# Kernel tuning notes

Measured on AMD Instinct MI355X. Metric: run time of the kernel, lower is better.

## Reference

```python
import jax, jax.numpy as jnp
import numpy as np

T = 4096          # num tokens
HID = 2048        # hidden_size
HQ = 32           # num q heads
HKV = 8           # num kv heads
G = HQ // HKV     # GQA group size
D = 128           # head_dim (q/k)
DV = 96           # v_head_dim
W = 512           # sliding window (= query block size)
THETA = 1e6
Q_SIZE, K_SIZE, V_SIZE = HQ * D, HKV * D, HKV * DV


def setup_inputs() -> dict:
    key = jax.random.key(0)
    k1, k2, k3, k4 = jax.random.split(key, 4)
    positions = jnp.arange(T, dtype=jnp.int32)
    hidden_states = jax.random.normal(k1, (T, HID), dtype=jnp.float32)
    qkv_w = jax.random.normal(k2, (Q_SIZE + K_SIZE + V_SIZE, HID), dtype=jnp.float32) * (HID ** -0.5)
    o_w = jax.random.normal(k3, (HID, HQ * DV), dtype=jnp.float32) * ((HQ * DV) ** -0.5)
    sink_bias = jax.random.normal(k4, (HQ,), dtype=jnp.float32)
    return {"positions": positions, "hidden_states": hidden_states,
            "qkv_w": qkv_w, "o_w": o_w, "sink_bias": sink_bias}


def _rope(x, positions):
    # neox-style rotate-half RoPE on full head_dim (partial_rotary_factor=1.0)
    half = D // 2
    inv_freq = 1.0 / (THETA ** (jnp.arange(0, half, dtype=jnp.float32) / half))
    ang = positions.astype(jnp.float32)[:, None] * inv_freq[None, :]   # [T, D/2]
    cos = jnp.cos(ang)[:, None, :]
    sin = jnp.sin(ang)[:, None, :]
    x1, x2 = x[..., :half], x[..., half:]
    return jnp.concatenate([x1 * cos - x2 * sin, x2 * cos + x1 * sin], axis=-1)


def _swa_with_sink(q, k, v, sink_bias):
    # q: [T, HKV, G, D], k: [T, HKV, D], v: [T, HKV, DV]
    nb = T // W
    scale = D ** -0.5
    qb = q.reshape(nb, W, HKV, G, D)
    # per query block i, keys/values from global span [(i-1)*W, (i+1)*W)
    k_pad = jnp.pad(k, ((W, 0), (0, 0), (0, 0)))
    v_pad = jnp.pad(v, ((W, 0), (0, 0), (0, 0)))
    idx = jnp.arange(nb)[:, None] * W + jnp.arange(2 * W)[None, :]     # [nb, 2W]
    k_ext = k_pad[idx]                                                 # [nb, 2W, HKV, D]
    v_ext = v_pad[idx]                                                 # [nb, 2W, HKV, DV]
    # mask: rel = t - j in [0, W); exclude left-pad keys (key_pos < 0)
    r = jnp.arange(W)[:, None]
    c = jnp.arange(2 * W)[None, :]
    rel = W + r - c                                                    # [W, 2W]
    key_pos = (jnp.arange(nb)[:, None, None] - 1) * W + c[None]        # [nb, W(1), 2W]
    mask = (rel >= 0) & (rel < W) & (key_pos >= 0)                     # [nb, W, 2W]
    scores = jnp.einsum('nrkgd,nckd->nkgrc', qb, k_ext) * scale        # [nb,HKV,G,W,2W]
    scores = jnp.where(mask[:, None, None, :, :], scores, -jnp.inf)
    sink = jnp.broadcast_to(sink_bias.reshape(HKV, G)[None, :, :, None, None],
                            (nb, HKV, G, W, 1))
    logits = jnp.concatenate([scores, sink], axis=-1)                  # [...,2W+1]
    p = jax.nn.softmax(logits, axis=-1)[..., :-1]                      # drop sink column
    out = jnp.einsum('nkgrc,nckd->nrkgd', p, v_ext)                    # [nb,W,HKV,G,DV]
    return out.reshape(T, HQ * DV)


def reference(positions, hidden_states, qkv_w, o_w, sink_bias):
    qkv = hidden_states @ qkv_w.T                                      # [T, Q+K+V]
    q, k, v = jnp.split(qkv, [Q_SIZE, Q_SIZE + K_SIZE], axis=-1)
    q = q.reshape(T, HQ, D)
    k = k.reshape(T, HKV, D)
    v = v.reshape(T, HKV, DV)
    q = _rope(q, positions).reshape(T, HKV, G, D)
    k = _rope(k, positions)
    attn = _swa_with_sink(q, k, v, sink_bias)                          # [T, HQ*DV]
    return attn @ o_w.T                                                # [T, HID]
```

## Files before the change

### kernel.cpp

```cpp
#include <hip/hip_runtime.h>
#include <hip/hip_bf16.h>
#include <stdint.h>

#define T_SEQ 4096
#define HIDDEN 2048
#define NQH 32
#define NKVH 8
#define DH 128
#define DVH 96
#define WWIN 512
#define QKVN 5888
#define KOFF 4096
#define VOFF 5120
#define ATTN 3072
#define QSCALE 0.08838834764831845f

typedef uint16_t u16;
typedef uint32_t u32;
typedef __bf16 bfrag8 __attribute__((ext_vector_type(8)));
typedef float f32x4v __attribute__((ext_vector_type(4)));

__device__ __forceinline__ u16 f2bf(float x) {
  u32 u = __float_as_uint(x);
  return (u16)((u + 0x7fffu + ((u >> 16) & 1u)) >> 16);
}
__device__ __forceinline__ float bf2f(u16 v) { return __uint_as_float(((u32)v) << 16); }

__global__ void cvt_kernel(const float* __restrict__ in, u16* __restrict__ out, int n4) {
  int i = blockIdx.x * blockDim.x + threadIdx.x;
  int st = gridDim.x * blockDim.x;
  for (; i < n4; i += st) {
    float4 v = ((const float4*)in)[i];
    ushort4 o;
    o.x = f2bf(v.x); o.y = f2bf(v.y); o.z = f2bf(v.z); o.w = f2bf(v.w);
    ((ushort4*)out)[i] = o;
  }
}

template<int OUT_F32>
__global__ __launch_bounds__(256) void gemm_nt(const u16* __restrict__ A,
                                               const u16* __restrict__ B,
                                               void* __restrict__ Cp,
                                               int M, int N, int K) {
  __shared__ u16 Asm[128 * 32];
  __shared__ u16 Bsm[128 * 32];
  const int tid = threadIdx.x;
  const int wv = tid >> 6, lane = tid & 63;
  const int bm = blockIdx.x * 128, bn = blockIdx.y * 128;
  const int wm = (wv >> 1) * 64, wn = (wv & 1) * 64;
  const int srow = lane >> 2;
  const int scol = (lane & 3) * 8;
  const int fr = lane & 15, fk = (lane >> 4) * 8;
  f32x4v acc[4][4];
#pragma unroll
  for (int i = 0; i < 4; i++)
#pragma unroll
    for (int j = 0; j < 4; j++) acc[i][j] = {0.f, 0.f, 0.f, 0.f};

  for (int kt = 0; kt < K; kt += 32) {
    __syncthreads();
#pragma unroll
    for (int c = 0; c < 2; c++) {
      const int ci = wv * 2 + c;
      const u16* ga = A + (size_t)(bm + ci * 16 + srow) * K + kt + scol;
      const u16* gb = B + (size_t)(bn + ci * 16 + srow) * K + kt + scol;
      __builtin_amdgcn_global_load_lds((const __attribute__((address_space(1))) u32*)ga,
                                       (__attribute__((address_space(3))) u32*)(Asm + ci * 512),
                                       16, 0, 0);
      __builtin_amdgcn_global_load_lds((const __attribute__((address_space(1))) u32*)gb,
                                       (__attribute__((address_space(3))) u32*)(Bsm + ci * 512),
                                       16, 0, 0);
    }
    __syncthreads();
    bfrag8 af[4], bf[4];
#pragma unroll
    for (int i = 0; i < 4; i++) af[i] = *(const bfrag8*)(Asm + (wm + i * 16 + fr) * 32 + fk);
#pragma unroll
    for (int j = 0; j < 4; j++) bf[j] = *(const bfrag8*)(Bsm + (wn + j * 16 + fr) * 32 + fk);
#pragma unroll
    for (int i = 0; i < 4; i++)
#pragma unroll
      for (int j = 0; j < 4; j++)
        acc[i][j] = __builtin_amdgcn_mfma_f32_16x16x32_bf16(af[i], bf[j], acc[i][j], 0, 0, 0);
  }
  const int orow = (lane >> 4) * 4, ocol = lane & 15;
#pragma unroll
  for (int i = 0; i < 4; i++)
#pragma unroll
    for (int j = 0; j < 4; j++) {
      size_t base = (size_t)(bm + wm + i * 16 + orow) * N + (size_t)(bn + wn + j * 16 + ocol);
#pragma unroll
      for (int r = 0; r < 4; r++) {
        if (OUT_F32) ((float*)Cp)[base + (size_t)r * N] = acc[i][j][r];
        else         ((u16*)Cp)[base + (size_t)r * N] = f2bf(acc[i][j][r]);
      }
    }
}

__global__ void rope_kernel(u16* __restrict__ qkv, const int* __restrict__ pos) {
  int gid = blockIdx.x * 256 + threadIdx.x;
  int d = gid & 63;
  int r = gid >> 6;
  int hh = r % 40;
  int t = r / 40;
  if (t >= T_SEQ) return;
  int off = (hh < 32) ? hh * 128 : KOFF + (hh - 32) * 128;
  u16* p = qkv + (size_t)t * QKVN + off + d;
  float x1 = bf2f(p[0]);
  float x2 = bf2f(p[64]);
  float inv_freq = exp2f(-(float)d * 0.3114307588956852f);
  float ang = (float)pos[t] * inv_freq;
  float c = cosf(ang), s = sinf(ang);
  float y1 = x1 * c - x2 * s;
  float y2 = x2 * c + x1 * s;
  if (hh < 32) { y1 *= QSCALE; y2 *= QSCALE; }
  p[0] = f2bf(y1);
  p[64] = f2bf(y2);
}

__global__ __launch_bounds__(256) void vt_kernel(const u16* __restrict__ qkv,
                                                 u16* __restrict__ vt) {
  __shared__ u16 tile[64][100];
  const int t0 = blockIdx.x * 64;
  const int hk = blockIdx.y;
  const int tid = threadIdx.x;
#pragma unroll
  for (int i = 0; i < 3; i++) {
    int idx = i * 256 + tid;
    int row = idx / 12, ch = idx % 12;
    const u16* g = qkv + (size_t)(t0 + row) * QKVN + VOFF + hk * DVH + ch * 8;
    uint2 a = *(const uint2*)g;
    uint2 b = *(const uint2*)(g + 4);
    *(uint2*)&tile[row][ch * 8] = a;
    *(uint2*)&tile[row][ch * 8 + 4] = b;
  }
  __syncthreads();
#pragma unroll
  for (int i = 0; i < 3; i++) {
    int idx = i * 256 + tid;
    int dv = idx >> 3, tc = (idx & 7) * 8;
    union { uint4 v4; u16 s[8]; } o;
#pragma unroll
    for (int j = 0; j < 8; j++) o.s[j] = tile[tc + j][dv];
    *(uint4*)(vt + (((size_t)(hk * 96 + dv)) << 12) + t0 + tc) = o.v4;
  }
}

__global__ __launch_bounds__(256, 2) void attn_mfma(const u16* __restrict__ qkv,
                                                    const u16* __restrict__ vt,
                                                    const float* __restrict__ sink_bias,
                                                    u16* __restrict__ attn_out) {
  __shared__ u16 k_lds[64 * 128];
  __shared__ u16 v_lds[96 * 64];
  __shared__ u16 p_lds[4][2048];

  const int tid = threadIdx.x;
  const int wv = tid >> 6;
  const int lane = tid & 63;
  const int g = lane >> 4;
  const int c = lane & 15;
  const int t0 = blockIdx.x * 32;
  const int hk = blockIdx.y;
  const int h = hk * 4 + wv;

  bfrag8 qf[2][4];
#pragma unroll
  for (int m = 0; m < 2; m++)
#pragma unroll
    for (int kf = 0; kf < 4; kf++)
      qf[m][kf] = *(const bfrag8*)(qkv + (size_t)(t0 + m * 16 + c) * QKVN + h * DH + kf * 32 + g * 8);

  f32x4v acc_o[2][6];
#pragma unroll
  for (int m = 0; m < 2; m++)
#pragma unroll
    for (int n = 0; n < 6; n++) acc_o[m][n] = {0.f, 0.f, 0.f, 0.f};

  const float sb = sink_bias[h];
  float m_run[2][4], l_run[2][4];
#pragma unroll
  for (int m = 0; m < 2; m++)
#pragma unroll
    for (int r = 0; r < 4; r++) { m_run[m][r] = sb; l_run[m][r] = 1.0f; }

  int cb0 = t0 - (WWIN - 1);
  cb0 = (cb0 < 0) ? 0 : (cb0 & ~63);

  for (int cb = cb0; cb < t0 + 32; cb += 64) {
    __syncthreads();
#pragma unroll
    for (int it = 0; it < 4; it++) {
      int dest = it * 4096 + tid * 16;
      int row = dest >> 8;
      int src = dest ^ ((row & 7) << 4);
      const u16* gp = qkv + (size_t)(cb + row) * QKVN + KOFF + hk * DH + ((src & 255) >> 1);
      __builtin_amdgcn_global_load_lds((const __attribute__((address_space(1))) u32*)gp,
                                       (__attribute__((address_space(3))) u32*)((char*)k_lds + dest),
                                       16, 0, 0);
    }
#pragma unroll
    for (int it = 0; it < 3; it++) {
      int dest = it * 4096 + tid * 16;
      int row = dest >> 7;
      int src = dest ^ ((row & 7) << 4);
      const u16* gp = vt + (((size_t)(hk * 96 + row)) << 12) + cb + ((src & 127) >> 1);
      __builtin_amdgcn_global_load_lds((const __attribute__((address_space(1))) u32*)gp,
                                       (__attribute__((address_space(3))) u32*)((char*)v_lds + dest),
                                       16, 0, 0);
    }
    __syncthreads();

    f32x4v s[2][4];
#pragma unroll
    for (int m = 0; m < 2; m++)
#pragma unroll
      for (int n = 0; n < 4; n++) s[m][n] = {0.f, 0.f, 0.f, 0.f};
#pragma unroll
    for (int kf = 0; kf < 4; kf++) {
      bfrag8 kb[4];
#pragma unroll
      for (int n = 0; n < 4; n++) {
        int key = n * 16 + c;
        int byt = ((key << 8) + (kf << 6) + (g << 4)) ^ ((key & 7) << 4);
        kb[n] = *(const bfrag8*)((const char*)k_lds + byt);
      }
#pragma unroll
      for (int m = 0; m < 2; m++)
#pragma unroll
        for (int n = 0; n < 4; n++)
          s[m][n] = __builtin_amdgcn_mfma_f32_16x16x32_bf16(qf[m][kf], kb[n], s[m][n], 0, 0, 0);
    }

    if ((cb + 63 > t0) || (cb + WWIN < t0 + 32)) {
#pragma unroll
      for (int m = 0; m < 2; m++)
#pragma unroll
        for (int n = 0; n < 4; n++)
#pragma unroll
          for (int r = 0; r < 4; r++) {
            int rel = (t0 + m * 16 + g * 4 + r) - (cb + n * 16 + c);
            if (!(rel >= 0 && rel < WWIN)) s[m][n][r] = -3.0e38f;
          }
    }

    float corr[2][4];
#pragma unroll
    for (int m = 0; m < 2; m++)
#pragma unroll
      for (int r = 0; r < 4; r++) {
        float v0 = fmaxf(fmaxf(s[m][0][r], s[m][1][r]), fmaxf(s[m][2][r], s[m][3][r]));
        v0 = fmaxf(v0, __shfl_xor(v0, 1));
        v0 = fmaxf(v0, __shfl_xor(v0, 2));
        v0 = fmaxf(v0, __shfl_xor(v0, 4));
        v0 = fmaxf(v0, __shfl_xor(v0, 8));
        float mn = fmaxf(m_run[m][r], v0);
        corr[m][r] = __expf(m_run[m][r] - mn);
        m_run[m][r] = mn;
        float p0 = __expf(s[m][0][r] - mn);
        float p1 = __expf(s[m][1][r] - mn);
        float p2 = __expf(s[m][2][r] - mn);
        float p3 = __expf(s[m][3][r] - mn);
        s[m][0][r] = p0; s[m][1][r] = p1; s[m][2][r] = p2; s[m][3][r] = p3;
        float rs = p0 + p1 + p2 + p3;
        rs += __shfl_xor(rs, 1);
        rs += __shfl_xor(rs, 2);
        rs += __shfl_xor(rs, 4);
        rs += __shfl_xor(rs, 8);
        l_run[m][r] = l_run[m][r] * corr[m][r] + rs;
      }
#pragma unroll
    for (int m = 0; m < 2; m++)
#pragma unroll
      for (int n = 0; n < 6; n++)
#pragma unroll
      for (int r = 0; r < 4; r++) acc_o[m][n][r] *= corr[m][r];

#pragma unroll
    for (int m = 0; m < 2; m++)
#pragma unroll
      for (int n = 0; n < 4; n++) {
        u32 lo = (u32)f2bf(s[m][n][0]) | ((u32)f2bf(s[m][n][1]) << 16);
        u32 hi = (u32)f2bf(s[m][n][2]) | ((u32)f2bf(s[m][n][3]) << 16);
        int byt = ((m * 2 + (n >> 1)) << 10) | (g << 3) | ((c & 3) << 5) |
                  (((c >> 2) & 1) << 9) | ((((n & 1) * 2) + (c >> 3)) << 7);
        uint2 u; u.x = lo; u.y = hi;
        *(uint2*)((char*)&p_lds[wv][0] + byt) = u;
      }

#pragma unroll
    for (int ks = 0; ks < 2; ks++) {
      bfrag8 pa[2];
#pragma unroll
      for (int m = 0; m < 2; m++) {
        union { bfrag8 v; u16 s16[8]; } u;
#pragma unroll
        for (int j = 0; j < 4; j++) {
          int e = ((m * 2 + ks) << 9) + c + j * 16 + g * 64;
          u.s16[j] = p_lds[wv][e];
          u.s16[4 + j] = p_lds[wv][e + 256];
        }
        pa[m] = u.v;
      }
#pragma unroll
      for (int n = 0; n < 6; n++) {
        int dv = n * 16 + c;
        int byt = ((dv << 7) + (ks << 6) + (g << 4)) ^ ((dv & 7) << 4);
        bfrag8 vb = *(const bfrag8*)((const char*)v_lds + byt);
#pragma unroll
        for (int m = 0; m < 2; m++)
          acc_o[m][n] = __builtin_amdgcn_mfma_f32_16x16x32_bf16(pa[m], vb, acc_o[m][n], 0, 0, 0);
      }
    }
  }

#pragma unroll
  for (int m = 0; m < 2; m++) {
    float inv[4];
#pragma unroll
    for (int r = 0; r < 4; r++) inv[r] = 1.0f / l_run[m][r];
#pragma unroll
    for (int n = 0; n < 6; n++)
#pragma unroll
      for (int r = 0; r < 4; r++) {
        int tq = t0 + m * 16 + g * 4 + r;
        attn_out[(size_t)tq * ATTN + h * DVH + n * 16 + c] = f2bf(acc_o[m][n][r] * inv[r]);
      }
  }
}

extern "C" void kernel_launch(void* const* d_in, const int* in_sizes, int n_in,
                              void* d_out, int out_size, void* d_ws, size_t ws_size,
                              hipStream_t stream) {
  const int* positions = (const int*)d_in[0];
  const float* hidden = (const float*)d_in[1];
  const float* qkv_w = (const float*)d_in[2];
  const float* o_w = (const float*)d_in[3];
  const float* sink = (const float*)d_in[4];
  char* ws = (char*)d_ws;

  u16* hs_bf   = (u16*)(ws + 0);
  u16* w1_bf   = (u16*)(ws + 16777216);
  u16* attn_bf = (u16*)(ws + 0);
  u16* vt_buf  = (u16*)(ws + 25165824);
  u16* w2_bf   = (u16*)(ws + 40894464);
  u16* qkv_bf  = (u16*)(ws + 53477376);

  cvt_kernel<<<dim3(1024), dim3(256), 0, stream>>>(hidden, hs_bf, 8388608 / 4);
  cvt_kernel<<<dim3(1024), dim3(256), 0, stream>>>(qkv_w, w1_bf, 12058624 / 4);
  cvt_kernel<<<dim3(1024), dim3(256), 0, stream>>>(o_w, w2_bf, 6291456 / 4);

  gemm_nt<0><<<dim3(32, 46), dim3(256), 0, stream>>>(hs_bf, w1_bf, (void*)qkv_bf,
                                                     T_SEQ, QKVN, HIDDEN);
  rope_kernel<<<dim3(40960), dim3(256), 0, stream>>>(qkv_bf, positions);
  vt_kernel<<<dim3(T_SEQ / 64, NKVH), dim3(256), 0, stream>>>(qkv_bf, vt_buf);
  attn_mfma<<<dim3(T_SEQ / 32, NKVH), dim3(256), 0, stream>>>(qkv_bf, vt_buf, sink, attn_bf);
  gemm_nt<1><<<dim3(32, 16), dim3(256), 0, stream>>>(attn_bf, w2_bf, d_out,
                                                     T_SEQ, HIDDEN, ATTN);
}
```

Before: 349.0 us.

## Add triple-buffered direct-to-LDS pipelined GEMM for QKV and output projections

Adds a new GEMM kernel with 512 threads and 256-row tiles. It uses global_load_lds to copy tiles straight into XOR-swizzled shared memory, keeps three buffers in flight with explicit vmcnt waits, raises wave priority around the MFMA blocks, and remaps workgroup IDs across XCDs. Both projection GEMMs use it, with a fallback to the old kernel if the dynamic LDS attribute cannot be set. The aim is to hide global memory latency and cut LDS bank conflicts and register-staging overhead, at the cost of large LDS use (up to 96KB) and more complex synchronisation.

```diff
diff --git a/kernel.cpp b/kernel.cpp
--- a/kernel.cpp
+++ b/kernel.cpp
@@ -35,6 +35,141 @@
     o.x = f2bf(v.x); o.y = f2bf(v.y); o.z = f2bf(v.z); o.w = f2bf(v.w);
     ((ushort4*)out)[i] = o;
   }
+}
+
+template<int WN, int OUT_F32>
+__global__ __launch_bounds__(512, 2) void gemm_pipe(const u16* __restrict__ A,
+                                                    const u16* __restrict__ B,
+                                                    void* __restrict__ Cp,
+                                                    int M, int N, int K, int nbm) {
+  constexpr int BN = WN * 64;
+  constexpr int WM = 8 / WN;
+  constexpr int MF = 16 / WM;
+  constexpr int ASZ = 8192;
+  constexpr int BSZ = BN * 32;
+  constexpr int BUFSZ = ASZ + BSZ;
+  constexpr int AIN = 2;
+  constexpr int BIN = (WN == 4) ? 2 : 1;
+  constexpr int LPT = AIN + BIN;
+
+  extern __shared__ u16 lds[];
+
+  const int tid = threadIdx.x;
+  const int w = tid >> 6, lane = tid & 63;
+  const int wr = w / WN, wc = w % WN;
+  const int fr = lane & 15, kg = lane >> 4;
+
+  const int nwg = gridDim.x;
+  int bid = (int)blockIdx.x;
+  if ((nwg & 7) == 0) bid = (bid & 7) * (nwg >> 3) + (bid >> 3);
+  const int bm = (bid % nbm) * 256;
+  const int bn = (bid / nbm) * BN;
+
+  const int NT = K >> 5;
+
+  f32x4v acc[MF][4];
+#pragma unroll
+  for (int m = 0; m < MF; m++)
+#pragma unroll
+    for (int n = 0; n < 4; n++) acc[m][n] = {0.f, 0.f, 0.f, 0.f};
+
+  auto stageA = [&](int t) {
+    u16* dst = lds + (t % 3) * BUFSZ;
+#pragma unroll
+    for (int i = 0; i < AIN; i++) {
+      int D = (w * AIN + i) * 1024 + lane * 16;
+      int srow = D >> 7;
+      int Dx = D ^ ((srow & 7) << 4);
+      int c = (Dx >> 1) & 63;
+      int m = 2 * srow + (c >> 5);
+      int k = c & 31;
+      const u16* src = A + (size_t)(bm + m) * K + (t << 5) + k;
+      __builtin_amdgcn_global_load_lds((const __attribute__((address_space(1))) u32*)src,
+                                       (__attribute__((address_space(3))) u32*)((char*)dst + D),
+                                       16, 0, 0);
+    }
+  };
+  auto stageB = [&](int t) {
+    u16* dst = lds + (t % 3) * BUFSZ + ASZ;
+#pragma unroll
+    for (int i = 0; i < BIN; i++) {
+      int D = (w * BIN + i) * 1024 + lane * 16;
+      int srow = D >> 7;
+      int Dx = D ^ ((srow & 7) << 4);
+      int c = (Dx >> 1) & 63;
+      int m = 2 * srow + (c >> 5);
+      int k = c & 31;
+      const u16* src = B + (size_t)(bn + m) * K + (t << 5) + k;
+      __builtin_amdgcn_global_load_lds((const __attribute__((address_space(1))) u32*)src,
+                                       (__attribute__((address_space(3))) u32*)((char*)dst + D),
+                                       16, 0, 0);
+    }
+  };
+
+  stageA(0); stageB(0);
+  stageA(1); stageB(1);
+
+  for (int t = 0; t < NT; ++t) {
+    const u16* At = lds + (t % 3) * BUFSZ;
+    const u16* Bt = At + ASZ;
+    if (t + 1 < NT) asm volatile("s_waitcnt vmcnt(%0)" :: "n"(LPT));
+    else            asm volatile("s_waitcnt vmcnt(0)");
+    asm volatile("s_barrier" ::: "memory");
+
+    bfrag8 bfr[4];
+#pragma unroll
+    for (int n = 0; n < 4; n++) {
+      int nr = wc * 64 + n * 16 + fr;
+      int byt = (((nr >> 1) << 7) + ((nr & 1) << 6) + (kg << 4)) ^ (((nr >> 1) & 7) << 4);
+      bfr[n] = *(const bfrag8*)((const char*)Bt + byt);
+    }
+    bfrag8 afr[MF / 2];
+#pragma unroll
+    for (int m = 0; m < MF / 2; m++) {
+      int mr = wr * (MF * 16) + m * 16 + fr;
+      int byt = (((mr >> 1) << 7) + ((mr & 1) << 6) + (kg << 4)) ^ (((mr >> 1) & 7) << 4);
+      afr[m] = *(const bfrag8*)((const char*)At + byt);
+    }
+    if (t + 2 < NT) stageA(t + 2);
+    __builtin_amdgcn_s_setprio(1);
+#pragma unroll
+    for (int m = 0; m < MF / 2; m++)
+#pragma unroll
+      for (int n = 0; n < 4; n++)
+        acc[m][n] = __builtin_amdgcn_mfma_f32_16x16x32_bf16(afr[m], bfr[n], acc[m][n], 0, 0, 0);
+    __builtin_amdgcn_s_setprio(0);
+    asm volatile("s_barrier" ::: "memory");
+
+    bfrag8 afr2[MF / 2];
+#pragma unroll
+    for (int m = 0; m < MF / 2; m++) {
+      int mr = wr * (MF * 16) + (m + MF / 2) * 16 + fr;
+      int byt = (((mr >> 1) << 7) + ((mr & 1) << 6) + (kg << 4)) ^ (((mr >> 1) & 7) << 4);
+      afr2[m] = *(const bfrag8*)((const char*)At + byt);
+    }
+    if (t + 2 < NT) stageB(t + 2);
+    __builtin_amdgcn_s_setprio(1);
+#pragma unroll
+    for (int m = 0; m < MF / 2; m++)
+#pragma unroll
+      for (int n = 0; n < 4; n++)
+        acc[m + MF / 2][n] = __builtin_amdgcn_mfma_f32_16x16x32_bf16(afr2[m], bfr[n], acc[m + MF / 2][n], 0, 0, 0);
+    __builtin_amdgcn_s_setprio(0);
+  }
+
+  const int rb = bm + wr * (MF * 16);
+  const int cb = bn + wc * 64;
+#pragma unroll
+  for (int m = 0; m < MF; m++)
+#pragma unroll
+    for (int n = 0; n < 4; n++) {
+      size_t base = (size_t)(rb + m * 16 + kg * 4) * N + cb + n * 16 + fr;
+#pragma unroll
+      for (int r = 0; r < 4; r++) {
+        if (OUT_F32) ((float*)Cp)[base + (size_t)r * N] = acc[m][n][r];
+        else         ((u16*)Cp)[base + (size_t)r * N] = f2bf(acc[m][n][r]);
+      }
+    }
 }
 
 template<int OUT_F32>
@@ -345,15 +480,31 @@
   u16* w2_bf   = (u16*)(ws + 40894464);
   u16* qkv_bf  = (u16*)(ws + 53477376);
 
+  bool pipeOk =
+    (hipFuncSetAttribute((const void*)&gemm_pipe<4, 0>,
+                         hipFuncAttributeMaxDynamicSharedMemorySize, 98304) == hipSuccess) &&
+    (hipFuncSetAttribute((const void*)&gemm_pipe<2, 1>,
+                         hipFuncAttributeMaxDynamicSharedMemorySize, 73728) == hipSuccess);
+
   cvt_kernel<<<dim3(1024), dim3(256), 0, stream>>>(hidden, hs_bf, 8388608 / 4);
   cvt_kernel<<<dim3(1024), dim3(256), 0, stream>>>(qkv_w, w1_bf, 12058624 / 4);
   cvt_kernel<<<dim3(1024), dim3(256), 0, stream>>>(o_w, w2_bf, 6291456 / 4);
 
-  gemm_nt<0><<<dim3(32, 46), dim3(256), 0, stream>>>(hs_bf, w1_bf, (void*)qkv_bf,
-                                                     T_SEQ, QKVN, HIDDEN);
+  if (pipeOk)
+    gemm_pipe<4, 0><<<dim3(368), dim3(512), 98304, stream>>>(hs_bf, w1_bf, (void*)qkv_bf,
+                                                             T_SEQ, QKVN, HIDDEN, 16);
+  else
+    gemm_nt<0><<<dim3(32, 46), dim3(256), 0, stream>>>(hs_bf, w1_bf, (void*)qkv_bf,
+                                                       T_SEQ, QKVN, HIDDEN);
+
   rope_kernel<<<dim3(40960), dim3(256), 0, stream>>>(qkv_bf, positions);
   vt_kernel<<<dim3(T_SEQ / 64, NKVH), dim3(256), 0, stream>>>(qkv_bf, vt_buf);
   attn_mfma<<<dim3(T_SEQ / 32, NKVH), dim3(256), 0, stream>>>(qkv_bf, vt_buf, sink, attn_bf);
-  gemm_nt<1><<<dim3(32, 16), dim3(256), 0, stream>>>(attn_bf, w2_bf, d_out,
-                                                     T_SEQ, HIDDEN, ATTN);
-}
+
+  if (pipeOk)
+    gemm_pipe<2, 1><<<dim3(256), dim3(512), 73728, stream>>>(attn_bf, w2_bf, d_out,
+                                                             T_SEQ, HIDDEN, ATTN, 16);
+  else
+    gemm_nt<1><<<dim3(32, 16), dim3(256), 0, stream>>>(attn_bf, w2_bf, d_out,
+                                                       T_SEQ, HIDDEN, ATTN);
+}
```

After: 322.8 us. 7.5% less time.

## Add triple-buffered 256x128 GEMM with 32x32 MFMA for both projections

Applied to the files above, without the earlier changes.

Adds a new GEMM kernel with 256x128 tiles, 512 threads, and K-steps of 64. It triple-buffers LDS tiles loaded asynchronously with global_load_lds, using a swizzled layout and a partial vmcnt wait so the next tile's load overlaps compute. It also uses the 32x32x16 MFMA, s_setprio around the MFMA bursts, and an XCD-aware block remap. The QKV and output projections use it when 144KB of dynamic LDS can be set, and fall back to the old kernel otherwise. In exchange it needs a large LDS footprint (with launch_bounds(512,2)) and does a hipFuncSetAttribute call on every launch.

```diff
diff --git a/kernel.cpp b/kernel.cpp
--- a/kernel.cpp
+++ b/kernel.cpp
@@ -19,12 +19,18 @@
 typedef uint32_t u32;
 typedef __bf16 bfrag8 __attribute__((ext_vector_type(8)));
 typedef float f32x4v __attribute__((ext_vector_type(4)));
+typedef float f32x16 __attribute__((ext_vector_type(16)));
 
 __device__ __forceinline__ u16 f2bf(float x) {
   u32 u = __float_as_uint(x);
   return (u16)((u + 0x7fffu + ((u >> 16) & 1u)) >> 16);
 }
 __device__ __forceinline__ float bf2f(u16 v) { return __uint_as_float(((u32)v) << 16); }
+
+__device__ __forceinline__ void gload16(const u16* src, char* ldst) {
+  __builtin_amdgcn_global_load_lds((const __attribute__((address_space(1))) u32*)src,
+                                   (__attribute__((address_space(3))) u32*)ldst, 16, 0, 0);
+}
 
 __global__ void cvt_kernel(const float* __restrict__ in, u16* __restrict__ out, int n4) {
   int i = blockIdx.x * blockDim.x + threadIdx.x;
@@ -35,6 +41,127 @@
     o.x = f2bf(v.x); o.y = f2bf(v.y); o.z = f2bf(v.z); o.w = f2bf(v.w);
     ((ushort4*)out)[i] = o;
   }
+}
+
+template<int OUT_F32>
+__global__ __launch_bounds__(512, 2) void gemm_v3(const u16* __restrict__ A,
+                                                  const u16* __restrict__ B,
+                                                  void* __restrict__ Cp,
+                                                  int M, int N, int K, int nbm) {
+  extern __shared__ char lds[];
+  const int tid = threadIdx.x;
+  const int w = tid >> 6, lane = tid & 63;
+  const int wr = w >> 1, wc = w & 1;
+  const int r5 = lane & 31, kg = lane >> 5;
+
+  const int nwg = gridDim.x;
+  int bid = (int)blockIdx.x;
+  if ((nwg & 7) == 0) bid = (bid & 7) * (nwg >> 3) + (bid >> 3);
+  const int bm = (bid % nbm) * 256;
+  const int bn = (bid / nbm) * 128;
+  const int NT = K >> 6;
+
+  f32x16 acc[2][2];
+#pragma unroll
+  for (int mb = 0; mb < 2; mb++)
+#pragma unroll
+    for (int nb = 0; nb < 2; nb++)
+#pragma unroll
+      for (int i = 0; i < 16; i++) acc[mb][nb][i] = 0.f;
+
+  const int q = r5 * 128 + ((kg ^ (r5 & 7)) << 4);
+
+  auto stageA = [&](int t) {
+    char* dst = lds + (t % 3) * 49152;
+    const u16* Abase = A + (size_t)bm * K + ((size_t)t << 6);
+#pragma unroll
+    for (int i = 0; i < 4; i++) {
+      int D = (w * 4 + i) * 1024 + lane * 16;
+      int row = D >> 7;
+      int kb = (D ^ ((row & 7) << 4)) & 127;
+      gload16(Abase + (size_t)row * K + (kb >> 1), dst + D);
+    }
+  };
+  auto stageB = [&](int t) {
+    char* dst = lds + (t % 3) * 49152 + 32768;
+    const u16* Bbase = B + (size_t)bn * K + ((size_t)t << 6);
+#pragma unroll
+    for (int i = 0; i < 2; i++) {
+      int D = (w * 2 + i) * 1024 + lane * 16;
+      int row = D >> 7;
+      int kb = (D ^ ((row & 7) << 4)) & 127;
+      gload16(Bbase + (size_t)row * K + (kb >> 1), dst + D);
+    }
+  };
+
+  stageA(0); stageB(0);
+
+  for (int t = 0; t < NT; ++t) {
+    const char* Ab = lds + (t % 3) * 49152 + wr * 8192;
+    const char* Bb = lds + (t % 3) * 49152 + 32768 + wc * 8192;
+    if (t + 1 < NT) {
+      stageA(t + 1);
+      stageB(t + 1);
+      asm volatile("s_waitcnt vmcnt(6)");
+    } else {
+      asm volatile("s_waitcnt vmcnt(0)");
+    }
+    asm volatile("s_barrier" ::: "memory");
+
+    bfrag8 af[2][2], bf[2][2];
+#pragma unroll
+    for (int ks = 0; ks < 2; ks++) {
+#pragma unroll
+      for (int mb = 0; mb < 2; mb++)
+        af[mb][ks] = *(const bfrag8*)(Ab + mb * 4096 + (q ^ (ks << 5)));
+#pragma unroll
+      for (int nb = 0; nb < 2; nb++)
+        bf[nb][ks] = *(const bfrag8*)(Bb + nb * 4096 + (q ^ (ks << 5)));
+    }
+    __builtin_amdgcn_s_setprio(1);
+#pragma unroll
+    for (int ks = 0; ks < 2; ks++)
+#pragma unroll
+      for (int mb = 0; mb < 2; mb++)
+#pragma unroll
+        for (int nb = 0; nb < 2; nb++)
+          acc[mb][nb] = __builtin_amdgcn_mfma_f32_32x32x16_bf16(af[mb][ks], bf[nb][ks], acc[mb][nb], 0, 0, 0);
+    __builtin_amdgcn_s_setprio(0);
+
+    bfrag8 af2[2][2], bf2[2][2];
+#pragma unroll
+    for (int ks = 0; ks < 2; ks++) {
+#pragma unroll
+      for (int mb = 0; mb < 2; mb++)
+        af2[mb][ks] = *(const bfrag8*)(Ab + mb * 4096 + (q ^ ((ks + 2) << 5)));
+#pragma unroll
+      for (int nb = 0; nb < 2; nb++)
+        bf2[nb][ks] = *(const bfrag8*)(Bb + nb * 4096 + (q ^ ((ks + 2) << 5)));
+    }
+    __builtin_amdgcn_s_setprio(1);
+#pragma unroll
+    for (int ks = 0; ks < 2; ks++)
+#pragma unroll
+      for (int mb = 0; mb < 2; mb++)
+#pragma unroll
+        for (int nb = 0; nb < 2; nb++)
+          acc[mb][nb] = __builtin_amdgcn_mfma_f32_32x32x16_bf16(af2[mb][ks], bf2[nb][ks], acc[mb][nb], 0, 0, 0);
+    __builtin_amdgcn_s_setprio(0);
+  }
+
+  const int rb0 = bm + wr * 64;
+  const int cb0 = bn + wc * 64;
+#pragma unroll
+  for (int mb = 0; mb < 2; mb++)
+#pragma unroll
+    for (int nb = 0; nb < 2; nb++)
+#pragma unroll
+      for (int i = 0; i < 16; i++) {
+        int rowl = (i & 3) + 8 * (i >> 2) + 4 * kg;
+        size_t off = (size_t)(rb0 + mb * 32 + rowl) * N + cb0 + nb * 32 + r5;
+        if (OUT_F32) ((float*)Cp)[off] = acc[mb][nb][i];
+        else         ((u16*)Cp)[off] = f2bf(acc[mb][nb][i]);
+      }
 }
 
 template<int OUT_F32>
@@ -64,12 +191,8 @@
       const int ci = wv * 2 + c;
       const u16* ga = A + (size_t)(bm + ci * 16 + srow) * K + kt + scol;
       const u16* gb = B + (size_t)(bn + ci * 16 + srow) * K + kt + scol;
-      __builtin_amdgcn_global_load_lds((const __attribute__((address_space(1))) u32*)ga,
-                                       (__attribute__((address_space(3))) u32*)(Asm + ci * 512),
-                                       16, 0, 0);
-      __builtin_amdgcn_global_load_lds((const __attribute__((address_space(1))) u32*)gb,
-                                       (__attribute__((address_space(3))) u32*)(Bsm + ci * 512),
-                                       16, 0, 0);
+      gload16(ga, (char*)(Asm + ci * 512));
+      gload16(gb, (char*)(Bsm + ci * 512));
     }
     __syncthreads();
     bfrag8 af[4], bf[4];
@@ -194,9 +317,7 @@
       int row = dest >> 8;
       int src = dest ^ ((row & 7) << 4);
       const u16* gp = qkv + (size_t)(cb + row) * QKVN + KOFF + hk * DH + ((src & 255) >> 1);
-      __builtin_amdgcn_global_load_lds((const __attribute__((address_space(1))) u32*)gp,
-                                       (__attribute__((address_space(3))) u32*)((char*)k_lds + dest),
-                                       16, 0, 0);
+      gload16(gp, (char*)k_lds + dest);
     }
 #pragma unroll
     for (int it = 0; it < 3; it++) {
@@ -204,9 +325,7 @@
       int row = dest >> 7;
       int src = dest ^ ((row & 7) << 4);
       const u16* gp = vt + (((size_t)(hk * 96 + row)) << 12) + cb + ((src & 127) >> 1);
-      __builtin_amdgcn_global_load_lds((const __attribute__((address_space(1))) u32*)gp,
-                                       (__attribute__((address_space(3))) u32*)((char*)v_lds + dest),
-                                       16, 0, 0);
+      gload16(gp, (char*)v_lds + dest);
     }
     __syncthreads();
 
@@ -345,15 +464,31 @@
   u16* w2_bf   = (u16*)(ws + 40894464);
   u16* qkv_bf  = (u16*)(ws + 53477376);
 
+  bool v3Ok =
+    (hipFuncSetAttribute((const void*)&gemm_v3<0>,
+                         hipFuncAttributeMaxDynamicSharedMemorySize, 147456) == hipSuccess) &&
+    (hipFuncSetAttribute((const void*)&gemm_v3<1>,
+                         hipFuncAttributeMaxDynamicSharedMemorySize, 147456) == hipSuccess);
+
   cvt_kernel<<<dim3(1024), dim3(256), 0, stream>>>(hidden, hs_bf, 8388608 / 4);
   cvt_kernel<<<dim3(1024), dim3(256), 0, stream>>>(qkv_w, w1_bf, 12058624 / 4);
   cvt_kernel<<<dim3(1024), dim3(256), 0, stream>>>(o_w, w2_bf, 6291456 / 4);
 
-  gemm_nt<0><<<dim3(32, 46), dim3(256), 0, stream>>>(hs_bf, w1_bf, (void*)qkv_bf,
-                                                     T_SEQ, QKVN, HIDDEN);
+  if (v3Ok)
+    gemm_v3<0><<<dim3(736), dim3(512), 147456, stream>>>(hs_bf, w1_bf, (void*)qkv_bf,
+                                                         T_SEQ, QKVN, HIDDEN, 16);
+  else
+    gemm_nt<0><<<dim3(32, 46), dim3(256), 0, stream>>>(hs_bf, w1_bf, (void*)qkv_bf,
+                                                       T_SEQ, QKVN, HIDDEN);
+
   rope_kernel<<<dim3(40960), dim3(256), 0, stream>>>(qkv_bf, positions);
   vt_kernel<<<dim3(T_SEQ / 64, NKVH), dim3(256), 0, stream>>>(qkv_bf, vt_buf);
   attn_mfma<<<dim3(T_SEQ / 32, NKVH), dim3(256), 0, stream>>>(qkv_bf, vt_buf, sink, attn_bf);
-  gemm_nt<1><<<dim3(32, 16), dim3(256), 0, stream>>>(attn_bf, w2_bf, d_out,
-                                                     T_SEQ, HIDDEN, ATTN);
-}
+
+  if (v3Ok)
+    gemm_v3<1><<<dim3(256), dim3(512), 147456, stream>>>(attn_bf, w2_bf, d_out,
+                                                         T_SEQ, HIDDEN, ATTN, 16);
+  else
+    gemm_nt<1><<<dim3(32, 16), dim3(256), 0, stream>>>(attn_bf, w2_bf, d_out,
+                                                       T_SEQ, HIDDEN, ATTN);
+}
```

New measurement: 312.4 us. 10.5% less time.
